# Optimization experiments

Hardware: AMD Instinct MI355X
Metric: run time of the kernel (lower is better)

## Reference

```python
import jax, jax.numpy as jnp
import numpy as np

B, S, D = 8, 2048, 512
UNITS = 512

def setup_inputs() -> dict:
    key = jax.random.key(0)
    k1, k2, k3, k4 = jax.random.split(key, 4)
    x = jax.random.normal(k1, (B, S, D), dtype=jnp.float32)
    # glorot-like scale for weights
    scale = 1.0 / np.sqrt(D)
    W_q = jax.random.normal(k2, (D, UNITS), dtype=jnp.float32) * scale
    W_k = jax.random.normal(k3, (D, UNITS), dtype=jnp.float32) * scale
    W_v = jax.random.normal(k4, (D, UNITS), dtype=jnp.float32) * scale
    return {"x": x, "W_q": W_q, "W_k": W_k, "W_v": W_v}

def reference(x, W_q, W_k, W_v):
    # Q,K,V: [B,S,U]
    Q = jnp.einsum('bsd,du->bsu', x, W_q)
    Km = jnp.einsum('bsd,du->bsu', x, W_k)
    V = jnp.einsum('bsd,du->bsu', x, W_v)
    units = W_q.shape[-1]
    # scores: [B,S,S] = Q @ K^T / sqrt(units)
    scores = jnp.einsum('bqu,bku->bqk', Q, Km) / jnp.sqrt(jnp.float32(units))
    attn = jax.nn.softmax(scores, axis=-1)
    # output: [B,S,U]
    return jnp.einsum('bqk,bku->bqu', attn, V)
```

## Files before the change

### kernel.cpp

```cpp
#include <hip/hip_runtime.h>
#include <math.h>

#define BN 8
#define SN 2048
#define DN 512
#define UN 512
#define MN (BN*SN)

typedef _Float16 f16;
typedef _Float16 f16x8 __attribute__((ext_vector_type(8)));
typedef _Float16 f16x4 __attribute__((ext_vector_type(4)));
typedef _Float16 f16x2 __attribute__((ext_vector_type(2)));
typedef float    f32x4 __attribute__((ext_vector_type(4)));

#define SCALE 0.044194173824159216f
#define LOG2E 1.4426950408889634f

#define CVT_PK(a, b) __builtin_bit_cast(f16x2, __builtin_amdgcn_cvt_pkrtz((a), (b)))

#define BAR_LGKM() do {                                         \
  asm volatile("s_waitcnt lgkmcnt(0)" ::: "memory");            \
  __builtin_amdgcn_s_barrier();                                 \
  __builtin_amdgcn_sched_barrier(0);                            \
} while (0)

__device__ __forceinline__ void gload_lds16(const f16* g, f16* l) {
  __builtin_amdgcn_global_load_lds(
      (const __attribute__((address_space(1))) unsigned int*)g,
      (__attribute__((address_space(3))) unsigned int*)l, 16, 0, 0);
}

__global__ __launch_bounds__(256) void cvt_x_kernel(const float* __restrict__ x,
                                                    f16* __restrict__ x16) {
  int i = (blockIdx.x * 256 + threadIdx.x) * 4;
  float4 v = *(const float4*)(x + i);
  f16x4 o = { (f16)v.x, (f16)v.y, (f16)v.z, (f16)v.w };
  *(f16x4*)(x16 + i) = o;
}

__global__ __launch_bounds__(256) void cvt_w_kernel(const float* __restrict__ Wq,
                                                    const float* __restrict__ Wk,
                                                    const float* __restrict__ Wv,
                                                    f16* __restrict__ Wt) {
  const float* W = blockIdx.y == 0 ? Wq : (blockIdx.y == 1 ? Wk : Wv);
  const float s = blockIdx.y == 0 ? SCALE : 1.0f;
  f16* o = Wt + (size_t)blockIdx.y * DN * UN;
  int t = blockIdx.x * 256 + threadIdx.x;
  int r  = t >> 7;
  int c4 = (t & 127) * 4;
  float4 v = *(const float4*)(W + (size_t)r * UN + c4);
  o[(size_t)(c4 + 0) * DN + r] = (f16)(v.x * s);
  o[(size_t)(c4 + 1) * DN + r] = (f16)(v.y * s);
  o[(size_t)(c4 + 2) * DN + r] = (f16)(v.z * s);
  o[(size_t)(c4 + 3) * DN + r] = (f16)(v.w * s);
}

__global__ __launch_bounds__(256) void qkv_gemm(const f16* __restrict__ x16,
                                                const f16* __restrict__ Wt,
                                                f16* __restrict__ Qh,
                                                f16* __restrict__ Kh,
                                                f16* __restrict__ Vt) {
  __shared__ __align__(16) f16 As[128 * 32];
  __shared__ __align__(16) f16 Bs[128 * 32];

  const int tid = threadIdx.x;
  const int w = tid >> 6, lane = tid & 63;
  const int l15 = lane & 15, lh = lane >> 4;
  const int m0 = blockIdx.x * 128;
  const int n0 = blockIdx.y * 128;
  const int widx = blockIdx.z;
  const f16* Wbase = Wt + (size_t)widx * DN * UN;

  const int wr = (w >> 1) * 64, wc = (w & 1) * 64;
  f32x4 acc[4][4] = {};

  for (int kk = 0; kk < 16; ++kk) {
    const int k0 = kk * 32;
#pragma unroll
    for (int q = 0; q < 2; ++q) {
      int j = q * 256 + tid;
      int r = j >> 2, cs = j & 3;
      int c = cs ^ ((r >> 1) & 3);
      f16* abase = &As[(q * 256 + w * 64) * 8];
      f16* bbase = &Bs[(q * 256 + w * 64) * 8];
      gload_lds16(x16 + (size_t)(m0 + r) * DN + k0 + c * 8, abase);
      gload_lds16(Wbase + (size_t)(n0 + r) * DN + k0 + c * 8, bbase);
    }
    __syncthreads();

    f16x8 a[4], bfr[4];
#pragma unroll
    for (int m = 0; m < 4; ++m) {
      int row = wr + m * 16 + l15;
      int ch = lh ^ ((row >> 1) & 3);
      a[m] = *(const f16x8*)&As[row * 32 + ch * 8];
    }
#pragma unroll
    for (int n = 0; n < 4; ++n) {
      int row = wc + n * 16 + l15;
      int ch = lh ^ ((row >> 1) & 3);
      bfr[n] = *(const f16x8*)&Bs[row * 32 + ch * 8];
    }
#pragma unroll
    for (int m = 0; m < 4; ++m)
#pragma unroll
      for (int n = 0; n < 4; ++n)
        acc[m][n] = __builtin_amdgcn_mfma_f32_16x16x32_f16(a[m], bfr[n], acc[m][n], 0, 0, 0);
    __syncthreads();
  }

  if (widx == 2) {
#pragma unroll
    for (int m = 0; m < 4; ++m) {
      int g = m0 + wr + m * 16 + lh * 4;
      int bb = g >> 11;
      int ss = g & 2047;
#pragma unroll
      for (int n = 0; n < 4; ++n) {
        int u = n0 + wc + n * 16 + l15;
        f16x4 pv = { (f16)acc[m][n][0], (f16)acc[m][n][1],
                     (f16)acc[m][n][2], (f16)acc[m][n][3] };
        *(f16x4*)(Vt + ((size_t)bb * UN + u) * SN + ss) = pv;
      }
    }
  } else {
    f16* O = (widx == 0) ? Qh : Kh;
#pragma unroll
    for (int m = 0; m < 4; ++m)
#pragma unroll
      for (int n = 0; n < 4; ++n)
#pragma unroll
        for (int j = 0; j < 4; ++j)
          O[(size_t)(m0 + wr + m * 16 + lh * 4 + j) * UN + (n0 + wc + n * 16 + l15)] =
              (f16)acc[m][n][j];
  }
}

__global__ __launch_bounds__(512, 2) void attn_kernel(const f16* __restrict__ Qh,
                                                      const f16* __restrict__ Kh,
                                                      const f16* __restrict__ Vt,
                                                      float* __restrict__ out) {
  __shared__ __align__(16) f16 Ks[64 * 512];
  __shared__ __align__(16) f16 Ps[64 * 72];
  __shared__ float redm[2][4][16];
  __shared__ float redl[2][4][16];

  const int tid = threadIdx.x;
  const int w = tid >> 6, lane = tid & 63;
  const int l15 = lane & 15, lh = lane >> 4;
  const int bid = blockIdx.x;
  const int b = bid & 7;
  const int q0 = (bid >> 3) * 64;
  const int rb = w >> 1;
  const int cs = w & 1;

  const f16* Kbat = Kh + (size_t)b * SN * DN;
  const f16* Vbat = Vt + (size_t)b * UN * SN;

  const f16* Qbase = Qh + (size_t)(b * SN + q0 + rb * 16 + l15) * DN;
  f16x8 qf[16];
#pragma unroll
  for (int kc = 0; kc < 16; ++kc)
    qf[kc] = *(const f16x8*)(Qbase + kc * 32 + lh * 8);

  f32x4 acc[4][4] = {};
  float mj[4] = { -1e30f, -1e30f, -1e30f, -1e30f };
  float mrow = -1e30f, lrow = 0.f;

  const f16* vbase = Vbat + (size_t)(w * 64 + l15) * SN + lh * 8;

#pragma unroll
  for (int q = 0; q < 8; ++q) {
    int r = w * 8 + q;
    gload_lds16(Kbat + (size_t)r * DN + (lane ^ (r & 7)) * 8, &Ks[r * 512]);
  }
  f16x8 vreg[4][2];
#pragma unroll
  for (int ut = 0; ut < 4; ++ut)
#pragma unroll
    for (int ks = 0; ks < 2; ++ks)
      vreg[ut][ks] = *(const f16x8*)(vbase + (size_t)(ut * 16) * SN + ks * 32);
  asm volatile("s_waitcnt vmcnt(8)" ::: "memory");
  __builtin_amdgcn_s_barrier();
  __builtin_amdgcn_sched_barrier(0);

  const int kswz = l15 & 7;

  for (int t = 0; t < 32; ++t) {
    const int kv0 = t * 64;

    f32x4 sc0 = {}, sc1 = {};
    const int r0 = cs * 32 + l15;
    __builtin_amdgcn_s_setprio(1);
#pragma unroll
    for (int kc = 0; kc < 16; ++kc) {
      int ch = ((kc * 4 + lh) ^ kswz) * 8;
      f16x8 k0 = *(const f16x8*)&Ks[r0 * 512 + ch];
      f16x8 k1 = *(const f16x8*)&Ks[(r0 + 16) * 512 + ch];
      sc0 = __builtin_amdgcn_mfma_f32_16x16x32_f16(k0, qf[kc], sc0, 0, 0, 0);
      sc1 = __builtin_amdgcn_mfma_f32_16x16x32_f16(k1, qf[kc], sc1, 0, 0, 0);
    }
    __builtin_amdgcn_s_setprio(0);

    float pm = fmaxf(fmaxf(fmaxf(sc0[0], sc0[1]), fmaxf(sc0[2], sc0[3])),
                     fmaxf(fmaxf(sc1[0], sc1[1]), fmaxf(sc1[2], sc1[3])));
    pm = fmaxf(pm, __shfl_xor(pm, 16, 64));
    pm = fmaxf(pm, __shfl_xor(pm, 32, 64));
    if (lh == 0) redm[cs][rb][l15] = pm;
    BAR_LGKM();

    if (t < 31) {
#pragma unroll
      for (int q = 0; q < 8; ++q) {
        int r = w * 8 + q;
        gload_lds16(Kbat + (size_t)(kv0 + 64 + r) * DN + (lane ^ (r & 7)) * 8,
                    &Ks[r * 512]);
      }
    }

#pragma unroll
    for (int qt = 0; qt < 4; ++qt) {
      float mn = fmaxf(mj[qt], fmaxf(redm[0][qt][l15], redm[1][qt][l15]));
      float rs = exp2f((mj[qt] - mn) * LOG2E);
      mj[qt] = mn;
#pragma unroll
      for (int ut = 0; ut < 4; ++ut) {
        acc[ut][qt][0] *= rs; acc[ut][qt][1] *= rs;
        acc[ut][qt][2] *= rs; acc[ut][qt][3] *= rs;
      }
    }

    float mnr = mj[rb];
    float rsr = exp2f((mrow - mnr) * LOG2E);
    mrow = mnr;
    float p[8];
#pragma unroll
    for (int j = 0; j < 4; ++j) {
      p[j]     = exp2f((sc0[j] - mrow) * LOG2E);
      p[4 + j] = exp2f((sc1[j] - mrow) * LOG2E);
    }
    float ts = (p[0] + p[1]) + (p[2] + p[3]) + (p[4] + p[5]) + (p[6] + p[7]);
    ts += __shfl_xor(ts, 16, 64);
    ts += __shfl_xor(ts, 32, 64);
    lrow = lrow * rsr + ts;

    const int pbase = (rb * 16 + l15) * 72 + cs * 32 + lh * 4;
    *(f16x2*)&Ps[pbase +  0] = CVT_PK(p[0], p[1]);
    *(f16x2*)&Ps[pbase +  2] = CVT_PK(p[2], p[3]);
    *(f16x2*)&Ps[pbase + 16] = CVT_PK(p[4], p[5]);
    *(f16x2*)&Ps[pbase + 18] = CVT_PK(p[6], p[7]);
    BAR_LGKM();

    __builtin_amdgcn_s_setprio(1);
#pragma unroll
    for (int ks = 0; ks < 2; ++ks) {
#pragma unroll
      for (int qt = 0; qt < 4; ++qt) {
        f16x8 pf = *(const f16x8*)&Ps[(qt * 16 + l15) * 72 + ks * 32 + lh * 8];
#pragma unroll
        for (int ut = 0; ut < 4; ++ut)
          acc[ut][qt] = __builtin_amdgcn_mfma_f32_16x16x32_f16(vreg[ut][ks], pf,
                                                               acc[ut][qt], 0, 0, 0);
      }
    }
    __builtin_amdgcn_s_setprio(0);

    if (t < 31) {
#pragma unroll
      for (int ut = 0; ut < 4; ++ut)
#pragma unroll
        for (int ks = 0; ks < 2; ++ks)
          vreg[ut][ks] = *(const f16x8*)(vbase + (size_t)(ut * 16) * SN +
                                         kv0 + 64 + ks * 32);
      asm volatile("s_waitcnt vmcnt(8)" ::: "memory");
    } else {
      asm volatile("s_waitcnt vmcnt(0)" ::: "memory");
    }
    __builtin_amdgcn_s_barrier();
    __builtin_amdgcn_sched_barrier(0);
  }

  if (lh == 0) redl[cs][rb][l15] = lrow;
  __syncthreads();
#pragma unroll
  for (int qt = 0; qt < 4; ++qt) {
    float linv = 1.0f / (redl[0][qt][l15] + redl[1][qt][l15]);
    float* orow = out + (size_t)(b * SN + q0 + qt * 16 + l15) * UN + w * 64 + lh * 4;
#pragma unroll
    for (int ut = 0; ut < 4; ++ut) {
      f32x4 o = acc[ut][qt];
      o[0] *= linv; o[1] *= linv; o[2] *= linv; o[3] *= linv;
      *(f32x4*)(orow + ut * 16) = o;
    }
  }
}

extern "C" void kernel_launch(void* const* d_in, const int* in_sizes, int n_in,
                              void* d_out, int out_size, void* d_ws, size_t ws_size,
                              hipStream_t stream) {
  const float* x  = (const float*)d_in[0];
  const float* Wq = (const float*)d_in[1];
  const float* Wk = (const float*)d_in[2];
  const float* Wv = (const float*)d_in[3];
  float* out = (float*)d_out;

  f16* x16 = (f16*)d_ws;
  f16* Wt  = x16 + (size_t)MN * DN;
  f16* Qh  = Wt + (size_t)3 * DN * UN;
  f16* Kh  = Qh + (size_t)MN * UN;
  f16* Vt  = Kh + (size_t)MN * UN;

  cvt_x_kernel<<<dim3(MN * DN / 1024), 256, 0, stream>>>(x, x16);
  cvt_w_kernel<<<dim3(256, 3), 256, 0, stream>>>(Wq, Wk, Wv, Wt);
  qkv_gemm<<<dim3(128, 4, 3), 256, 0, stream>>>(x16, Wt, Qh, Kh, Vt);
  attn_kernel<<<256, 512, 0, stream>>>(Qh, Kh, Vt, out);
}
```

Before: 209.4 us.

## Double-buffer K tiles in LDS and remap score tiling for K reuse

K tiles now live in two LDS buffers. The prefetch of the next tile is issued at the start of each iteration into the idle buffer, so it overlaps the QK^T MFMAs instead of waiting behind the row-max barrier. The score work is also remapped: each wave covers 32 query rows by 16 keys and reuses one K fragment for two Q tiles, which halves K LDS reads per MFMA. The row-max and row-sum reductions become a 4-way layout read as one float4. In exchange, LDS use roughly doubles and the Q fragments held in registers double, which will likely stop two 512-thread blocks from sharing a CU and raises register pressure.

```diff
diff --git a/kernel.cpp b/kernel.cpp
--- a/kernel.cpp
+++ b/kernel.cpp
@@ -140,10 +140,10 @@
                                                       const f16* __restrict__ Kh,
                                                       const f16* __restrict__ Vt,
                                                       float* __restrict__ out) {
-  __shared__ __align__(16) f16 Ks[64 * 512];
+  __shared__ __align__(16) f16 Ks[2][64 * 512];
   __shared__ __align__(16) f16 Ps[64 * 72];
-  __shared__ float redm[2][4][16];
-  __shared__ float redl[2][4][16];
+  __shared__ __align__(16) float redm[64][4];
+  __shared__ __align__(16) float redl[64][4];
 
   const int tid = threadIdx.x;
   const int w = tid >> 6, lane = tid & 63;
@@ -151,28 +151,31 @@
   const int bid = blockIdx.x;
   const int b = bid & 7;
   const int q0 = (bid >> 3) * 64;
-  const int rb = w >> 1;
-  const int cs = w & 1;
+  const int rb = w >> 2;
+  const int cs = w & 3;
 
   const f16* Kbat = Kh + (size_t)b * SN * DN;
   const f16* Vbat = Vt + (size_t)b * UN * SN;
 
-  const f16* Qbase = Qh + (size_t)(b * SN + q0 + rb * 16 + l15) * DN;
-  f16x8 qf[16];
-#pragma unroll
-  for (int kc = 0; kc < 16; ++kc)
-    qf[kc] = *(const f16x8*)(Qbase + kc * 32 + lh * 8);
+  f16x8 qf[2][16];
+#pragma unroll
+  for (int qt = 0; qt < 2; ++qt) {
+    const f16* Qbase = Qh + (size_t)(b * SN + q0 + rb * 32 + qt * 16 + l15) * DN;
+#pragma unroll
+    for (int kc = 0; kc < 16; ++kc)
+      qf[qt][kc] = *(const f16x8*)(Qbase + kc * 32 + lh * 8);
+  }
 
   f32x4 acc[4][4] = {};
   float mj[4] = { -1e30f, -1e30f, -1e30f, -1e30f };
-  float mrow = -1e30f, lrow = 0.f;
+  float lrow[2] = { 0.f, 0.f };
 
   const f16* vbase = Vbat + (size_t)(w * 64 + l15) * SN + lh * 8;
 
 #pragma unroll
   for (int q = 0; q < 8; ++q) {
     int r = w * 8 + q;
-    gload_lds16(Kbat + (size_t)r * DN + (lane ^ (r & 7)) * 8, &Ks[r * 512]);
+    gload_lds16(Kbat + (size_t)r * DN + (lane ^ (r & 7)) * 8, &Ks[0][r * 512]);
   }
   f16x8 vreg[4][2];
 #pragma unroll
@@ -187,80 +190,83 @@
   const int kswz = l15 & 7;
 
   for (int t = 0; t < 32; ++t) {
+    const int cur = t & 1;
     const int kv0 = t * 64;
-
-    f32x4 sc0 = {}, sc1 = {};
-    const int r0 = cs * 32 + l15;
-    __builtin_amdgcn_s_setprio(1);
-#pragma unroll
-    for (int kc = 0; kc < 16; ++kc) {
-      int ch = ((kc * 4 + lh) ^ kswz) * 8;
-      f16x8 k0 = *(const f16x8*)&Ks[r0 * 512 + ch];
-      f16x8 k1 = *(const f16x8*)&Ks[(r0 + 16) * 512 + ch];
-      sc0 = __builtin_amdgcn_mfma_f32_16x16x32_f16(k0, qf[kc], sc0, 0, 0, 0);
-      sc1 = __builtin_amdgcn_mfma_f32_16x16x32_f16(k1, qf[kc], sc1, 0, 0, 0);
-    }
-    __builtin_amdgcn_s_setprio(0);
-
-    float pm = fmaxf(fmaxf(fmaxf(sc0[0], sc0[1]), fmaxf(sc0[2], sc0[3])),
-                     fmaxf(fmaxf(sc1[0], sc1[1]), fmaxf(sc1[2], sc1[3])));
-    pm = fmaxf(pm, __shfl_xor(pm, 16, 64));
-    pm = fmaxf(pm, __shfl_xor(pm, 32, 64));
-    if (lh == 0) redm[cs][rb][l15] = pm;
-    BAR_LGKM();
 
     if (t < 31) {
 #pragma unroll
       for (int q = 0; q < 8; ++q) {
         int r = w * 8 + q;
         gload_lds16(Kbat + (size_t)(kv0 + 64 + r) * DN + (lane ^ (r & 7)) * 8,
-                    &Ks[r * 512]);
+                    &Ks[cur ^ 1][r * 512]);
       }
     }
 
-#pragma unroll
-    for (int qt = 0; qt < 4; ++qt) {
-      float mn = fmaxf(mj[qt], fmaxf(redm[0][qt][l15], redm[1][qt][l15]));
-      float rs = exp2f((mj[qt] - mn) * LOG2E);
-      mj[qt] = mn;
+    f32x4 sc0 = {}, sc1 = {};
+    const int krow = cs * 16 + l15;
+    __builtin_amdgcn_s_setprio(1);
+#pragma unroll
+    for (int kc = 0; kc < 16; ++kc) {
+      f16x8 kf = *(const f16x8*)&Ks[cur][krow * 512 + (((kc * 4 + lh) ^ kswz) * 8)];
+      sc0 = __builtin_amdgcn_mfma_f32_16x16x32_f16(kf, qf[0][kc], sc0, 0, 0, 0);
+      sc1 = __builtin_amdgcn_mfma_f32_16x16x32_f16(kf, qf[1][kc], sc1, 0, 0, 0);
+    }
+    __builtin_amdgcn_s_setprio(0);
+
+    float pm0 = fmaxf(fmaxf(sc0[0], sc0[1]), fmaxf(sc0[2], sc0[3]));
+    float pm1 = fmaxf(fmaxf(sc1[0], sc1[1]), fmaxf(sc1[2], sc1[3]));
+    pm0 = fmaxf(pm0, __shfl_xor(pm0, 16, 64));
+    pm0 = fmaxf(pm0, __shfl_xor(pm0, 32, 64));
+    pm1 = fmaxf(pm1, __shfl_xor(pm1, 16, 64));
+    pm1 = fmaxf(pm1, __shfl_xor(pm1, 32, 64));
+    if (lh == 0) {
+      redm[rb * 32 + l15][cs] = pm0;
+      redm[rb * 32 + 16 + l15][cs] = pm1;
+    }
+    BAR_LGKM();
+
+    float rs[4];
+#pragma unroll
+    for (int qt4 = 0; qt4 < 4; ++qt4) {
+      f32x4 m4 = *(const f32x4*)&redm[qt4 * 16 + l15][0];
+      float mn = fmaxf(fmaxf(fmaxf(m4[0], m4[1]), fmaxf(m4[2], m4[3])), mj[qt4]);
+      rs[qt4] = exp2f((mj[qt4] - mn) * LOG2E);
+      mj[qt4] = mn;
 #pragma unroll
       for (int ut = 0; ut < 4; ++ut) {
-        acc[ut][qt][0] *= rs; acc[ut][qt][1] *= rs;
-        acc[ut][qt][2] *= rs; acc[ut][qt][3] *= rs;
+        acc[ut][qt4][0] *= rs[qt4]; acc[ut][qt4][1] *= rs[qt4];
+        acc[ut][qt4][2] *= rs[qt4]; acc[ut][qt4][3] *= rs[qt4];
       }
     }
 
-    float mnr = mj[rb];
-    float rsr = exp2f((mrow - mnr) * LOG2E);
-    mrow = mnr;
-    float p[8];
-#pragma unroll
-    for (int j = 0; j < 4; ++j) {
-      p[j]     = exp2f((sc0[j] - mrow) * LOG2E);
-      p[4 + j] = exp2f((sc1[j] - mrow) * LOG2E);
-    }
-    float ts = (p[0] + p[1]) + (p[2] + p[3]) + (p[4] + p[5]) + (p[6] + p[7]);
-    ts += __shfl_xor(ts, 16, 64);
-    ts += __shfl_xor(ts, 32, 64);
-    lrow = lrow * rsr + ts;
-
-    const int pbase = (rb * 16 + l15) * 72 + cs * 32 + lh * 4;
-    *(f16x2*)&Ps[pbase +  0] = CVT_PK(p[0], p[1]);
-    *(f16x2*)&Ps[pbase +  2] = CVT_PK(p[2], p[3]);
-    *(f16x2*)&Ps[pbase + 16] = CVT_PK(p[4], p[5]);
-    *(f16x2*)&Ps[pbase + 18] = CVT_PK(p[6], p[7]);
+#pragma unroll
+    for (int qt = 0; qt < 2; ++qt) {
+      const int qi = rb * 2 + qt;
+      f32x4 s = qt == 0 ? sc0 : sc1;
+      float p0 = exp2f((s[0] - mj[qi]) * LOG2E);
+      float p1 = exp2f((s[1] - mj[qi]) * LOG2E);
+      float p2 = exp2f((s[2] - mj[qi]) * LOG2E);
+      float p3 = exp2f((s[3] - mj[qi]) * LOG2E);
+      float ts = (p0 + p1) + (p2 + p3);
+      ts += __shfl_xor(ts, 16, 64);
+      ts += __shfl_xor(ts, 32, 64);
+      lrow[qt] = lrow[qt] * rs[qi] + ts;
+      f16x2 lo = CVT_PK(p0, p1), hi = CVT_PK(p2, p3);
+      f16x4 pv = { lo[0], lo[1], hi[0], hi[1] };
+      *(f16x4*)&Ps[(rb * 32 + qt * 16 + l15) * 72 + cs * 16 + lh * 4] = pv;
+    }
     BAR_LGKM();
 
     __builtin_amdgcn_s_setprio(1);
 #pragma unroll
     for (int ks = 0; ks < 2; ++ks) {
 #pragma unroll
-      for (int qt = 0; qt < 4; ++qt) {
-        f16x8 pf = *(const f16x8*)&Ps[(qt * 16 + l15) * 72 + ks * 32 + lh * 8];
+      for (int qt4 = 0; qt4 < 4; ++qt4) {
+        f16x8 pf = *(const f16x8*)&Ps[(qt4 * 16 + l15) * 72 + ks * 32 + lh * 8];
 #pragma unroll
         for (int ut = 0; ut < 4; ++ut)
-          acc[ut][qt] = __builtin_amdgcn_mfma_f32_16x16x32_f16(vreg[ut][ks], pf,
-                                                               acc[ut][qt], 0, 0, 0);
+          acc[ut][qt4] = __builtin_amdgcn_mfma_f32_16x16x32_f16(vreg[ut][ks], pf,
+                                                                acc[ut][qt4], 0, 0, 0);
       }
     }
     __builtin_amdgcn_s_setprio(0);
@@ -280,15 +286,19 @@
     __builtin_amdgcn_sched_barrier(0);
   }
 
-  if (lh == 0) redl[cs][rb][l15] = lrow;
+  if (lh == 0) {
+    redl[rb * 32 + l15][cs] = lrow[0];
+    redl[rb * 32 + 16 + l15][cs] = lrow[1];
+  }
   __syncthreads();
 #pragma unroll
-  for (int qt = 0; qt < 4; ++qt) {
-    float linv = 1.0f / (redl[0][qt][l15] + redl[1][qt][l15]);
-    float* orow = out + (size_t)(b * SN + q0 + qt * 16 + l15) * UN + w * 64 + lh * 4;
+  for (int qt4 = 0; qt4 < 4; ++qt4) {
+    f32x4 l4 = *(const f32x4*)&redl[qt4 * 16 + l15][0];
+    float linv = 1.0f / ((l4[0] + l4[1]) + (l4[2] + l4[3]));
+    float* orow = out + (size_t)(b * SN + q0 + qt4 * 16 + l15) * UN + w * 64 + lh * 4;
 #pragma unroll
     for (int ut = 0; ut < 4; ++ut) {
-      f32x4 o = acc[ut][qt];
+      f32x4 o = acc[ut][qt4];
       o[0] *= linv; o[1] *= linv; o[2] *= linv; o[3] *= linv;
       *(f32x4*)(orow + ut * 16) = o;
     }
```

Result: slower. 283.9 us (+35.6%).

## Double KV tile to 128 and defer softmax rescaling below threshold

Applied to the files above, without the earlier changes.

The attention loop now processes 128 keys per iteration instead of 64. This halves the iteration count and the barriers and max reductions that come with it. It also adds lazy online-softmax rescaling: the accumulator is rescaled only when some lane's running max grows by more than a threshold. LDS use roughly doubles (128 KB of K plus a larger P buffer), and the V register buffer doubles. With launch_bounds(512,2) this likely drops occupancy to one block per CU and raises register pressure.

```diff
diff --git a/kernel.cpp b/kernel.cpp
--- a/kernel.cpp
+++ b/kernel.cpp
@@ -15,6 +15,7 @@
 
 #define SCALE 0.044194173824159216f
 #define LOG2E 1.4426950408889634f
+#define DEFER_THR 8.0f
 
 #define CVT_PK(a, b) __builtin_bit_cast(f16x2, __builtin_amdgcn_cvt_pkrtz((a), (b)))
 
@@ -140,8 +141,8 @@
                                                       const f16* __restrict__ Kh,
                                                       const f16* __restrict__ Vt,
                                                       float* __restrict__ out) {
-  __shared__ __align__(16) f16 Ks[64 * 512];
-  __shared__ __align__(16) f16 Ps[64 * 72];
+  __shared__ __align__(16) f16 Ks[128 * 512];
+  __shared__ __align__(16) f16 Ps[64 * 136];
   __shared__ float redm[2][4][16];
   __shared__ float redl[2][4][16];
 
@@ -170,93 +171,103 @@
   const f16* vbase = Vbat + (size_t)(w * 64 + l15) * SN + lh * 8;
 
 #pragma unroll
-  for (int q = 0; q < 8; ++q) {
-    int r = w * 8 + q;
+  for (int q = 0; q < 16; ++q) {
+    int r = w * 16 + q;
     gload_lds16(Kbat + (size_t)r * DN + (lane ^ (r & 7)) * 8, &Ks[r * 512]);
   }
-  f16x8 vreg[4][2];
+  f16x8 vreg[4][4];
 #pragma unroll
   for (int ut = 0; ut < 4; ++ut)
 #pragma unroll
-    for (int ks = 0; ks < 2; ++ks)
+    for (int ks = 0; ks < 4; ++ks)
       vreg[ut][ks] = *(const f16x8*)(vbase + (size_t)(ut * 16) * SN + ks * 32);
-  asm volatile("s_waitcnt vmcnt(8)" ::: "memory");
+  asm volatile("s_waitcnt vmcnt(16)" ::: "memory");
   __builtin_amdgcn_s_barrier();
   __builtin_amdgcn_sched_barrier(0);
 
   const int kswz = l15 & 7;
 
-  for (int t = 0; t < 32; ++t) {
-    const int kv0 = t * 64;
-
-    f32x4 sc0 = {}, sc1 = {};
-    const int r0 = cs * 32 + l15;
+  for (int t = 0; t < 16; ++t) {
+    const int kv0 = t * 128;
+
+    f32x4 sc[4] = {};
+    const int r0 = cs * 64 + l15;
     __builtin_amdgcn_s_setprio(1);
 #pragma unroll
     for (int kc = 0; kc < 16; ++kc) {
       int ch = ((kc * 4 + lh) ^ kswz) * 8;
-      f16x8 k0 = *(const f16x8*)&Ks[r0 * 512 + ch];
-      f16x8 k1 = *(const f16x8*)&Ks[(r0 + 16) * 512 + ch];
-      sc0 = __builtin_amdgcn_mfma_f32_16x16x32_f16(k0, qf[kc], sc0, 0, 0, 0);
-      sc1 = __builtin_amdgcn_mfma_f32_16x16x32_f16(k1, qf[kc], sc1, 0, 0, 0);
+#pragma unroll
+      for (int G = 0; G < 4; ++G) {
+        f16x8 kf = *(const f16x8*)&Ks[(r0 + G * 16) * 512 + ch];
+        sc[G] = __builtin_amdgcn_mfma_f32_16x16x32_f16(kf, qf[kc], sc[G], 0, 0, 0);
+      }
     }
     __builtin_amdgcn_s_setprio(0);
 
-    float pm = fmaxf(fmaxf(fmaxf(sc0[0], sc0[1]), fmaxf(sc0[2], sc0[3])),
-                     fmaxf(fmaxf(sc1[0], sc1[1]), fmaxf(sc1[2], sc1[3])));
+    float pm = -1e30f;
+#pragma unroll
+    for (int G = 0; G < 4; ++G)
+      pm = fmaxf(pm, fmaxf(fmaxf(sc[G][0], sc[G][1]), fmaxf(sc[G][2], sc[G][3])));
     pm = fmaxf(pm, __shfl_xor(pm, 16, 64));
     pm = fmaxf(pm, __shfl_xor(pm, 32, 64));
     if (lh == 0) redm[cs][rb][l15] = pm;
     BAR_LGKM();
 
-    if (t < 31) {
-#pragma unroll
-      for (int q = 0; q < 8; ++q) {
-        int r = w * 8 + q;
-        gload_lds16(Kbat + (size_t)(kv0 + 64 + r) * DN + (lane ^ (r & 7)) * 8,
+    if (t < 15) {
+#pragma unroll
+      for (int q = 0; q < 16; ++q) {
+        int r = w * 16 + q;
+        gload_lds16(Kbat + (size_t)(kv0 + 128 + r) * DN + (lane ^ (r & 7)) * 8,
                     &Ks[r * 512]);
       }
     }
 
+    float mn[4];
+    bool need = false;
 #pragma unroll
     for (int qt = 0; qt < 4; ++qt) {
-      float mn = fmaxf(mj[qt], fmaxf(redm[0][qt][l15], redm[1][qt][l15]));
-      float rs = exp2f((mj[qt] - mn) * LOG2E);
-      mj[qt] = mn;
-#pragma unroll
-      for (int ut = 0; ut < 4; ++ut) {
-        acc[ut][qt][0] *= rs; acc[ut][qt][1] *= rs;
-        acc[ut][qt][2] *= rs; acc[ut][qt][3] *= rs;
+      mn[qt] = fmaxf(mj[qt], fmaxf(redm[0][qt][l15], redm[1][qt][l15]));
+      need = need || (mn[qt] > mj[qt] + DEFER_THR);
+    }
+    if (__any(need)) {
+#pragma unroll
+      for (int qt = 0; qt < 4; ++qt) {
+        float rs = exp2f((mj[qt] - mn[qt]) * LOG2E);
+        mj[qt] = mn[qt];
+#pragma unroll
+        for (int ut = 0; ut < 4; ++ut) {
+          acc[ut][qt][0] *= rs; acc[ut][qt][1] *= rs;
+          acc[ut][qt][2] *= rs; acc[ut][qt][3] *= rs;
+        }
       }
     }
 
     float mnr = mj[rb];
     float rsr = exp2f((mrow - mnr) * LOG2E);
     mrow = mnr;
-    float p[8];
-#pragma unroll
-    for (int j = 0; j < 4; ++j) {
-      p[j]     = exp2f((sc0[j] - mrow) * LOG2E);
-      p[4 + j] = exp2f((sc1[j] - mrow) * LOG2E);
-    }
-    float ts = (p[0] + p[1]) + (p[2] + p[3]) + (p[4] + p[5]) + (p[6] + p[7]);
+    float ts = 0.f;
+#pragma unroll
+    for (int G = 0; G < 4; ++G) {
+      float p0 = exp2f((sc[G][0] - mrow) * LOG2E);
+      float p1 = exp2f((sc[G][1] - mrow) * LOG2E);
+      float p2 = exp2f((sc[G][2] - mrow) * LOG2E);
+      float p3 = exp2f((sc[G][3] - mrow) * LOG2E);
+      ts += (p0 + p1) + (p2 + p3);
+      f16x2 lo = CVT_PK(p0, p1), hi = CVT_PK(p2, p3);
+      f16x4 pv = { lo[0], lo[1], hi[0], hi[1] };
+      *(f16x4*)&Ps[(rb * 16 + l15) * 136 + cs * 64 + G * 16 + lh * 4] = pv;
+    }
     ts += __shfl_xor(ts, 16, 64);
     ts += __shfl_xor(ts, 32, 64);
     lrow = lrow * rsr + ts;
-
-    const int pbase = (rb * 16 + l15) * 72 + cs * 32 + lh * 4;
-    *(f16x2*)&Ps[pbase +  0] = CVT_PK(p[0], p[1]);
-    *(f16x2*)&Ps[pbase +  2] = CVT_PK(p[2], p[3]);
-    *(f16x2*)&Ps[pbase + 16] = CVT_PK(p[4], p[5]);
-    *(f16x2*)&Ps[pbase + 18] = CVT_PK(p[6], p[7]);
     BAR_LGKM();
 
     __builtin_amdgcn_s_setprio(1);
 #pragma unroll
-    for (int ks = 0; ks < 2; ++ks) {
+    for (int ks = 0; ks < 4; ++ks) {
 #pragma unroll
       for (int qt = 0; qt < 4; ++qt) {
-        f16x8 pf = *(const f16x8*)&Ps[(qt * 16 + l15) * 72 + ks * 32 + lh * 8];
+        f16x8 pf = *(const f16x8*)&Ps[(qt * 16 + l15) * 136 + ks * 32 + lh * 8];
 #pragma unroll
         for (int ut = 0; ut < 4; ++ut)
           acc[ut][qt] = __builtin_amdgcn_mfma_f32_16x16x32_f16(vreg[ut][ks], pf,
@@ -265,14 +276,14 @@
     }
     __builtin_amdgcn_s_setprio(0);
 
-    if (t < 31) {
+    if (t < 15) {
 #pragma unroll
       for (int ut = 0; ut < 4; ++ut)
 #pragma unroll
-        for (int ks = 0; ks < 2; ++ks)
+        for (int ks = 0; ks < 4; ++ks)
           vreg[ut][ks] = *(const f16x8*)(vbase + (size_t)(ut * 16) * SN +
-                                         kv0 + 64 + ks * 32);
-      asm volatile("s_waitcnt vmcnt(8)" ::: "memory");
+                                         kv0 + 128 + ks * 32);
+      asm volatile("s_waitcnt vmcnt(16)" ::: "memory");
     } else {
       asm volatile("s_waitcnt vmcnt(0)" ::: "memory");
     }
```

New measurement: 263.8 us. +26.0%, slower.
